# Performance work log

Measured on AMD Instinct MI355X. Metric: run time of the kernel, lower is better.

Reference implementation:

```python
import math
import jax, jax.numpy as jnp
import numpy as np

NH = 16          # num attention heads
NOPE = 128       # qk_nope_head_dim
ROPE = 64        # qk_rope_head_dim
VD = 128         # v_head_dim
QLR = 1536       # q_lora_rank
IH = 8           # index_n_heads
ID = 128         # index_head_dim
TOPK = 8         # index_topk
EPS = 1e-5


def layernorm(x, w, b):
    mu = jnp.mean(x, axis=-1, keepdims=True)
    var = jnp.mean((x - mu) ** 2, axis=-1, keepdims=True)
    return (x - mu) * jax.lax.rsqrt(var + EPS) * w + b


def rope_tables(dim, end, base=10000.0):
    freqs = 1.0 / (base ** (jnp.arange(0, dim, 2, dtype=jnp.float32) / dim))  # [dim//2]
    t = jnp.arange(end, dtype=jnp.float32)
    f = jnp.outer(t, freqs)  # [end, dim//2]
    return jnp.cos(f), jnp.sin(f)


def apply_rope(x, cos, sin):
    # x: [b, h, s, d]; cos/sin: [s, d//2] (interleaved real/imag pairs)
    xr, xi = x[..., 0::2], x[..., 1::2]
    c = cos[None, None, :, :]
    s = sin[None, None, :, :]
    or_, oi = xr * c - xi * s, xr * s + xi * c
    return jnp.stack([or_, oi], axis=-1).reshape(x.shape)


def setup_inputs() -> dict:
    key = jax.random.key(0)
    ks = jax.random.split(key, 16)
    H = 2048
    B, S = 2, 2048
    w = lambda k, shp: (jax.random.normal(k, shp, dtype=jnp.float32) * 0.02)
    return {
        "x": jax.random.normal(ks[0], (B, S, H), dtype=jnp.float32),
        "W_cq": w(ks[1], (H, QLR)),
        "q_norm_w": jnp.ones((QLR,), jnp.float32),
        "q_norm_b": jnp.zeros((QLR,), jnp.float32),
        "W_q": w(ks[2], (QLR, NH * (NOPE + ROPE))),
        "W_ckv": w(ks[3], (H, NH * (NOPE + ROPE))),
        "kv_norm_w": jnp.ones((NOPE,), jnp.float32),
        "kv_norm_b": jnp.zeros((NOPE,), jnp.float32),
        "W_kv": w(ks[4], (NOPE, NOPE + VD)),
        "W_o": w(ks[5], (NH * VD, H)),
        "W_ip": w(ks[6], (H, IH * ID)),
        "W_ig": w(ks[7], (H, IH)),
        "W_sq": w(ks[8], (ID, ID)),
        "W_sk": w(ks[9], (ID, ID)),
        "W_sv": w(ks[10], (ID, ID)),
        "W_io": w(ks[11], (ID, H)),
    }


def _forward(x, W_cq, q_norm_w, q_norm_b, W_q, W_ckv, kv_norm_w, kv_norm_b,
             W_kv, W_o, W_ip, W_ig, W_sq, W_sk, W_sv, W_io):
    B, S, H = x.shape
    # --- MLA dense path ---
    qc = layernorm(x @ W_cq, q_norm_w, q_norm_b)                  # [B,S,QLR]
    qp = (qc @ W_q).reshape(B, S, NH, NOPE + ROPE).transpose(0, 2, 1, 3)
    q_nope, q_pe = qp[..., :NOPE], qp[..., NOPE:]
    kvc = (x @ W_ckv).reshape(B, S, NH, ROPE + NOPE).transpose(0, 2, 1, 3)
    k_pe, kv_nope = kvc[..., :ROPE], kvc[..., ROPE:]
    kv_n = layernorm(kv_nope, kv_norm_w, kv_norm_b)               # [B,NH,S,NOPE]
    kvp = kv_n @ W_kv                                             # [B,NH,S,NOPE+VD]
    k_nope, v = kvp[..., :NOPE], kvp[..., NOPE:]
    cos, sin = rope_tables(ROPE, S)
    q_pe = apply_rope(q_pe, cos, sin)
    k_pe = apply_rope(k_pe, cos, sin)
    q = jnp.concatenate([q_nope, q_pe], axis=-1)                  # [B,NH,S,192]
    k = jnp.concatenate([k_nope, k_pe], axis=-1)
    scale = 1.0 / math.sqrt(NOPE + ROPE)
    scores = jnp.einsum("bhqd,bhkd->bhqk", q, k) * scale
    causal = jnp.triu(jnp.ones((S, S), dtype=bool), k=1)
    scores = jnp.where(causal[None, None], -jnp.inf, scores)
    probs = jax.nn.softmax(scores.astype(jnp.float32), axis=-1).astype(q.dtype)
    attn = jnp.einsum("bhqk,bhkd->bhqd", probs, v)                # [B,NH,S,VD]
    # --- NSA sparse path (lightning indexer) ---
    ist = (x @ W_ip).reshape(B, S, IH, ID).transpose(0, 2, 1, 3)  # [B,IH,S,ID]
    gate = (x @ W_ig).transpose(0, 2, 1)                          # [B,IH,S]
    _, top_idx = jax.lax.top_k(gate, TOPK)                        # [B,IH,TOPK]
    sel = jnp.take_along_axis(ist, top_idx[..., None], axis=2)    # [B,IH,TOPK,ID]
    sq, sk, sv = sel @ W_sq, sel @ W_sk, sel @ W_sv
    ss = jnp.einsum("bhqd,bhkd->bhqk", sq, sk) / math.sqrt(ID)    # [B,IH,TOPK,TOPK]
    sp = jax.nn.softmax(ss.astype(jnp.float32), axis=-1).astype(sq.dtype)
    so = jnp.einsum("bhqk,bhkd->bhqd", sp, sv)                    # [B,IH,TOPK,ID]
    sparse_out = so @ W_io                                        # [B,IH,TOPK,H]
    io = sparse_out.mean(axis=2)[:, :, None, :VD]                 # [B,IH,1,VD]
    io = jnp.broadcast_to(io, (B, IH, S, VD))
    io = jnp.repeat(io, NH // IH, axis=1)                         # [B,NH,S,VD]
    attn = attn + io
    out = attn.transpose(0, 2, 1, 3).reshape(B, S, NH * VD) @ W_o
    return out


def reference(x, W_cq, q_norm_w, q_norm_b, W_q, W_ckv, kv_norm_w, kv_norm_b,
              W_kv, W_o, W_ip, W_ig, W_sq, W_sk, W_sv, W_io):
    return _forward(x, W_cq, q_norm_w, q_norm_b, W_q, W_ckv, kv_norm_w,
                    kv_norm_b, W_kv, W_o, W_ip, W_ig, W_sq, W_sk, W_sv, W_io)
```

## Files before the change

kernel.cpp:

```cpp
#include <hip/hip_runtime.h>
#include <hip/hip_bf16.h>
#include <math.h>

#define NH    16
#define NOPE  128
#define ROPED 64
#define VD    128
#define QLR   1536
#define IH    8
#define ID    128
#define TOPK  8
#define EPSF  1e-5f
#define B_    2
#define S_    2048
#define H_    2048

using bf16 = __hip_bfloat16;
typedef __attribute__((ext_vector_type(8))) short short8;
typedef __attribute__((ext_vector_type(4))) short short4v;
typedef __attribute__((ext_vector_type(4))) float f32x4;

#define GLOBAL_AS __attribute__((address_space(1)))
#define LDS_AS    __attribute__((address_space(3)))

__device__ __forceinline__ float b2f(bf16 v) { return __bfloat162float(v); }
__device__ __forceinline__ bf16 f2b(float v) { return __float2bfloat16(v); }
__device__ __forceinline__ void stoC(float* p, float v) { *p = v; }
__device__ __forceinline__ void stoC(bf16* p, float v) { *p = __float2bfloat16(v); }

__global__ __launch_bounds__(256) void gate_k(const float* __restrict__ x,
                                              const float* __restrict__ Wg,
                                              float* __restrict__ gate) {
    const int t = threadIdx.x;
    const int wid = t >> 6, lane = t & 63;
    const int row = blockIdx.x * 4 + wid;
    const float* xp = x + (size_t)row * H_;

    float acc[8] = {};
    for (int k0 = 0; k0 < H_; k0 += 256) {
        const int kb = k0 + lane * 4;
        const f32x4 xv = *(const f32x4*)(xp + kb);
        const f32x4 w0 = *(const f32x4*)(Wg + (size_t)kb * 8);
        const f32x4 w1 = *(const f32x4*)(Wg + (size_t)kb * 8 + 4);
        const f32x4 w2 = *(const f32x4*)(Wg + (size_t)(kb + 1) * 8);
        const f32x4 w3 = *(const f32x4*)(Wg + (size_t)(kb + 1) * 8 + 4);
        const f32x4 w4 = *(const f32x4*)(Wg + (size_t)(kb + 2) * 8);
        const f32x4 w5 = *(const f32x4*)(Wg + (size_t)(kb + 2) * 8 + 4);
        const f32x4 w6 = *(const f32x4*)(Wg + (size_t)(kb + 3) * 8);
        const f32x4 w7 = *(const f32x4*)(Wg + (size_t)(kb + 3) * 8 + 4);
#pragma unroll
        for (int j = 0; j < 4; j++) {
            acc[j]     += xv[0] * w0[j] + xv[1] * w2[j] + xv[2] * w4[j] + xv[3] * w6[j];
            acc[4 + j] += xv[0] * w1[j] + xv[1] * w3[j] + xv[2] * w5[j] + xv[3] * w7[j];
        }
    }
#pragma unroll
    for (int j = 0; j < 8; j++) {
#pragma unroll
        for (int off = 32; off > 0; off >>= 1)
            acc[j] += __shfl_xor(acc[j], off);
    }
    if (lane == 0) {
#pragma unroll
        for (int j = 0; j < 8; j++) gate[(size_t)row * 8 + j] = acc[j];
    }
}

template <typename OT>
__global__ __launch_bounds__(256) void gemm_bt_mfma_k(const bf16* __restrict__ A,
                                                      const bf16* __restrict__ Bt,
                                                      OT* __restrict__ C,
                                                      int M, int N, int K) {
    __shared__ bf16 As[128 * 32];
    __shared__ bf16 Bs[128 * 32];
    const int t = threadIdx.x;
    const int w = t >> 6;
    const int l = t & 63;
    const int col = l & 15;
    const int quad = l >> 4;
    const int wm = w >> 1, wn = w & 1;
    const int row0 = blockIdx.y * 128;
    const int col0 = blockIdx.x * 128;

    const int rA = l >> 2;
    const int cA = (l & 3) * 8;
    const bf16* ga0 = A + (size_t)(row0 + w * 16 + rA) * K + cA;
    const bf16* ga1 = A + (size_t)(row0 + (4 + w) * 16 + rA) * K + cA;
    const bf16* gb0 = Bt + (size_t)(col0 + w * 16 + rA) * K + cA;
    const bf16* gb1 = Bt + (size_t)(col0 + (4 + w) * 16 + rA) * K + cA;
    bf16* lA0 = &As[w * 512];
    bf16* lA1 = &As[(4 + w) * 512];
    bf16* lB0 = &Bs[w * 512];
    bf16* lB1 = &Bs[(4 + w) * 512];

    f32x4 acc[4][4];
#pragma unroll
    for (int i = 0; i < 4; i++)
#pragma unroll
        for (int j = 0; j < 4; j++) acc[i][j] = (f32x4){0.f, 0.f, 0.f, 0.f};

    for (int k0 = 0; k0 < K; k0 += 32) {
        __syncthreads();
        __builtin_amdgcn_global_load_lds((const GLOBAL_AS void*)(ga0 + k0),
                                         (LDS_AS void*)lA0, 16, 0, 0);
        __builtin_amdgcn_global_load_lds((const GLOBAL_AS void*)(ga1 + k0),
                                         (LDS_AS void*)lA1, 16, 0, 0);
        __builtin_amdgcn_global_load_lds((const GLOBAL_AS void*)(gb0 + k0),
                                         (LDS_AS void*)lB0, 16, 0, 0);
        __builtin_amdgcn_global_load_lds((const GLOBAL_AS void*)(gb1 + k0),
                                         (LDS_AS void*)lB1, 16, 0, 0);
        __syncthreads();

        short8 af[4], bfr[4];
#pragma unroll
        for (int i = 0; i < 4; i++) {
            af[i]  = *(const short8*)&As[(wm * 64 + i * 16 + col) * 32 + quad * 8];
            bfr[i] = *(const short8*)&Bs[(wn * 64 + i * 16 + col) * 32 + quad * 8];
        }
#pragma unroll
        for (int i = 0; i < 4; i++)
#pragma unroll
            for (int j = 0; j < 4; j++)
                acc[i][j] = __builtin_amdgcn_mfma_f32_16x16x32_bf16(af[i], bfr[j], acc[i][j], 0, 0, 0);
    }

#pragma unroll
    for (int i = 0; i < 4; i++)
#pragma unroll
        for (int j = 0; j < 4; j++)
#pragma unroll
            for (int r = 0; r < 4; r++) {
                const int gr = row0 + wm * 64 + i * 16 + quad * 4 + r;
                const int gc = col0 + wn * 64 + j * 16 + col;
                stoC(C + (size_t)gr * N + gc, acc[i][j][r]);
            }
}

__global__ __launch_bounds__(256) void gemm_kv_k(const bf16* __restrict__ A,
                                                 const bf16* __restrict__ Bt,
                                                 bf16* __restrict__ kvc,
                                                 bf16* __restrict__ Vb) {
    __shared__ bf16 As[128 * 32];
    __shared__ bf16 Bs[128 * 32];
    const int K = 128;
    const int t = threadIdx.x;
    const int w = t >> 6;
    const int l = t & 63;
    const int col = l & 15;
    const int quad = l >> 4;
    const int wm = w >> 1, wn = w & 1;
    const int row0 = blockIdx.y * 128;
    const int col0 = blockIdx.x * 128;

    const int rA = l >> 2;
    const int cA = (l & 3) * 8;
    const bf16* ga0 = A + (size_t)(row0 + w * 16 + rA) * K + cA;
    const bf16* ga1 = A + (size_t)(row0 + (4 + w) * 16 + rA) * K + cA;
    const bf16* gb0 = Bt + (size_t)(col0 + w * 16 + rA) * K + cA;
    const bf16* gb1 = Bt + (size_t)(col0 + (4 + w) * 16 + rA) * K + cA;
    bf16* lA0 = &As[w * 512];
    bf16* lA1 = &As[(4 + w) * 512];
    bf16* lB0 = &Bs[w * 512];
    bf16* lB1 = &Bs[(4 + w) * 512];

    f32x4 acc[4][4];
#pragma unroll
    for (int i = 0; i < 4; i++)
#pragma unroll
        for (int j = 0; j < 4; j++) acc[i][j] = (f32x4){0.f, 0.f, 0.f, 0.f};

    for (int k0 = 0; k0 < K; k0 += 32) {
        __syncthreads();
        __builtin_amdgcn_global_load_lds((const GLOBAL_AS void*)(ga0 + k0),
                                         (LDS_AS void*)lA0, 16, 0, 0);
        __builtin_amdgcn_global_load_lds((const GLOBAL_AS void*)(ga1 + k0),
                                         (LDS_AS void*)lA1, 16, 0, 0);
        __builtin_amdgcn_global_load_lds((const GLOBAL_AS void*)(gb0 + k0),
                                         (LDS_AS void*)lB0, 16, 0, 0);
        __builtin_amdgcn_global_load_lds((const GLOBAL_AS void*)(gb1 + k0),
                                         (LDS_AS void*)lB1, 16, 0, 0);
        __syncthreads();

        short8 af[4], bfr[4];
#pragma unroll
        for (int i = 0; i < 4; i++) {
            af[i]  = *(const short8*)&As[(wm * 64 + i * 16 + col) * 32 + quad * 8];
            bfr[i] = *(const short8*)&Bs[(wn * 64 + i * 16 + col) * 32 + quad * 8];
        }
#pragma unroll
        for (int i = 0; i < 4; i++)
#pragma unroll
            for (int j = 0; j < 4; j++)
                acc[i][j] = __builtin_amdgcn_mfma_f32_16x16x32_bf16(af[i], bfr[j], acc[i][j], 0, 0, 0);
    }

#pragma unroll
    for (int i = 0; i < 4; i++)
#pragma unroll
        for (int j = 0; j < 4; j++)
#pragma unroll
            for (int r = 0; r < 4; r++) {
                const int gr = row0 + wm * 64 + i * 16 + quad * 4 + r;
                const int gc = col0 + wn * 64 + j * 16 + col;
                const int bb = gr >> 15;
                const int ss = (gr >> 4) & (S_ - 1);
                const int hh = gr & (NH - 1);
                const bf16 v = f2b(acc[i][j][r]);
                if (gc < 128) kvc[(size_t)gr * 192 + gc] = v;
                else Vb[(((size_t)(bb * NH + hh)) * S_ + ss) * 128 + (gc - 128)] = v;
            }
}

__global__ __launch_bounds__(256) void kv_ln_k(bf16* __restrict__ kvc,
                                               const float* __restrict__ knw,
                                               const float* __restrict__ knb,
                                               bf16* __restrict__ kvn) {
    const int idx = blockIdx.x * 4 + (threadIdx.x >> 6);
    const int lane = threadIdx.x & 63;
    const int s = (idx >> 4) & (S_ - 1);
    const size_t base = (size_t)idx * 192;

    const float v0 = b2f(kvc[base + 64 + lane]);
    const float v1 = b2f(kvc[base + 128 + lane]);
    float xr = 0.f, xi = 0.f;
    if (lane < 32) { xr = b2f(kvc[base + 2 * lane]); xi = b2f(kvc[base + 2 * lane + 1]); }

    float s1 = v0 + v1, s2 = v0 * v0 + v1 * v1;
#pragma unroll
    for (int off = 32; off > 0; off >>= 1) {
        s1 += __shfl_xor(s1, off);
        s2 += __shfl_xor(s2, off);
    }
    const float mu = s1 * (1.f / 128.f);
    const float rinv = rsqrtf(s2 * (1.f / 128.f) - mu * mu + EPSF);
    kvn[(size_t)idx * 128 + lane]      = f2b((v0 - mu) * rinv * knw[lane] + knb[lane]);
    kvn[(size_t)idx * 128 + lane + 64] = f2b((v1 - mu) * rinv * knw[lane + 64] + knb[lane + 64]);

    if (lane < 32) {
        const float freq = powf(10000.f, -(float)(2 * lane) / 64.f);
        const float ang = (float)s * freq;
        float sn, c; sincosf(ang, &sn, &c);
        kvc[base + 128 + 2 * lane]     = f2b(xr * c - xi * sn);
        kvc[base + 128 + 2 * lane + 1] = f2b(xr * sn + xi * c);
    }
}

__global__ __launch_bounds__(256) void cast_bf16_k(const float* __restrict__ X,
                                                   bf16* __restrict__ Y, int n4) {
    for (int i = blockIdx.x * 256 + threadIdx.x; i < n4; i += gridDim.x * 256) {
        const f32x4 v = ((const f32x4*)X)[i];
        short4v o;
#pragma unroll
        for (int j = 0; j < 4; j++) {
            bf16 b = f2b(v[j]);
            o[j] = *(short*)&b;
        }
        ((short4v*)Y)[i] = o;
    }
}

__global__ __launch_bounds__(256) void transpose_cast_k(const float* __restrict__ W,
                                                        bf16* __restrict__ Wt,
                                                        int K, int N) {
    __shared__ float tile[32][33];
    const int t = threadIdx.x;
    const int tx = t & 31, ty = t >> 5;
    const int n0 = blockIdx.x * 32;
    const int k0 = blockIdx.y * 32;
#pragma unroll
    for (int i = 0; i < 4; i++)
        tile[ty + 8 * i][tx] = W[(size_t)(k0 + ty + 8 * i) * N + n0 + tx];
    __syncthreads();
#pragma unroll
    for (int i = 0; i < 4; i++)
        Wt[(size_t)(n0 + ty + 8 * i) * K + k0 + tx] = f2b(tile[tx][ty + 8 * i]);
}

__global__ __launch_bounds__(256) void layernorm_cast_k(const float* __restrict__ X,
                                                        const float* __restrict__ w,
                                                        const float* __restrict__ b,
                                                        bf16* __restrict__ Y,
                                                        int L) {
    __shared__ float r1[256], r2[256];
    const int row = blockIdx.x;
    const int t = threadIdx.x;
    const float* xp = X + (size_t)row * L;
    bf16* yp = Y + (size_t)row * L;
    float s1 = 0.f, s2 = 0.f;
    for (int j = t; j < L; j += 256) { const float v = xp[j]; s1 += v; s2 += v * v; }
    r1[t] = s1; r2[t] = s2; __syncthreads();
    for (int off = 128; off > 0; off >>= 1) {
        if (t < off) { r1[t] += r1[t + off]; r2[t] += r2[t + off]; }
        __syncthreads();
    }
    const float mu   = r1[0] / (float)L;
    const float var  = r2[0] / (float)L - mu * mu;
    const float rinv = rsqrtf(var + EPSF);
    for (int j = t; j < L; j += 256)
        yp[j] = f2b((xp[j] - mu) * rinv * w[j] + b[j]);
}

__global__ __launch_bounds__(256) void q_rope_k(bf16* __restrict__ qp) {
    const int total = B_ * S_ * NH * 32;
    for (int p = blockIdx.x * 256 + threadIdx.x; p < total; p += gridDim.x * 256) {
        const int j = p & 31;
        const int row = p >> 5;
        const int sr = row >> 4;
        const int s = sr & (S_ - 1);
        const size_t base = (size_t)row * 192 + 128 + 2 * j;
        const float xr = b2f(qp[base]);
        const float xi = b2f(qp[base + 1]);
        const float freq = powf(10000.f, -(float)(2 * j) / 64.f);
        const float ang = (float)s * freq;
        float sn, c; sincosf(ang, &sn, &c);
        qp[base]     = f2b(xr * c - xi * sn);
        qp[base + 1] = f2b(xr * sn + xi * c);
    }
}

__global__ __launch_bounds__(256) void sparse_k(const float* __restrict__ gate,
                                                const float* __restrict__ ist,
                                                const float* __restrict__ Wsq,
                                                const float* __restrict__ Wsk,
                                                const float* __restrict__ Wsv,
                                                const float* __restrict__ Wio,
                                                float* __restrict__ io) {
    __shared__ float g[S_];
    __shared__ float sel[TOPK][ID];
    __shared__ float sq[TOPK][ID], sk[TOPK][ID], sv[TOPK][ID];
    __shared__ float sp[TOPK][TOPK];
    __shared__ float ms[ID];
    __shared__ float rv[256];
    __shared__ int ri[256];
    __shared__ int sidx[TOPK];
    const int bi = blockIdx.x;
    const int ih = bi % IH;
    const int b = bi / IH;
    const int t = threadIdx.x;

    for (int s = t; s < S_; s += 256) g[s] = gate[(size_t)(b * S_ + s) * IH + ih];
    __syncthreads();

    for (int r = 0; r < TOPK; r++) {
        float bv = -INFINITY; int bx = S_;
        for (int s = t; s < S_; s += 256) {
            const float v = g[s];
            if (v > bv) { bv = v; bx = s; }
        }
        rv[t] = bv; ri[t] = bx; __syncthreads();
        for (int off = 128; off > 0; off >>= 1) {
            if (t < off) {
                const float v2 = rv[t + off]; const int i2 = ri[t + off];
                if (v2 > rv[t] || (v2 == rv[t] && i2 < ri[t])) { rv[t] = v2; ri[t] = i2; }
            }
            __syncthreads();
        }
        if (t == 0) { sidx[r] = ri[0]; g[ri[0]] = -INFINITY; }
        __syncthreads();
    }

    for (int i = t; i < TOPK * ID; i += 256) {
        const int r = i >> 7, d = i & 127;
        sel[r][d] = ist[((size_t)(b * S_ + sidx[r]) * IH + ih) * ID + d];
    }
    __syncthreads();

    for (int i = t; i < TOPK * ID; i += 256) {
        const int r = i >> 7, n = i & 127;
        float aq = 0.f, ak = 0.f, av = 0.f;
        for (int k = 0; k < 128; k++) {
            const float s = sel[r][k];
            aq += s * Wsq[k * ID + n];
            ak += s * Wsk[k * ID + n];
            av += s * Wsv[k * ID + n];
        }
        sq[r][n] = aq; sk[r][n] = ak; sv[r][n] = av;
    }
    __syncthreads();

    if (t < TOPK * TOPK) {
        const int r = t >> 3, c = t & 7;
        float a = 0.f;
        for (int k = 0; k < 128; k++) a += sq[r][k] * sk[c][k];
        sp[r][c] = a * 0.08838834764831845f;
    }
    __syncthreads();

    if (t < TOPK) {
        float m = -INFINITY;
        for (int c = 0; c < 8; c++) m = fmaxf(m, sp[t][c]);
        float e[8]; float sum = 0.f;
        for (int c = 0; c < 8; c++) { e[c] = expf(sp[t][c] - m); sum += e[c]; }
        for (int c = 0; c < 8; c++) sp[t][c] = e[c] / sum;
    }
    __syncthreads();

    if (t < ID) {
        float acc = 0.f;
        for (int r = 0; r < 8; r++) {
            float so = 0.f;
            for (int c = 0; c < 8; c++) so += sp[r][c] * sv[c][t];
            acc += so;
        }
        ms[t] = acc * 0.125f;
    }
    __syncthreads();

    if (t < ID) {
        float acc = 0.f;
        for (int k = 0; k < 128; k++) acc += ms[k] * Wio[(size_t)k * H_ + t];
        io[((size_t)b * IH + ih) * ID + t] = acc;
    }
}

__global__ __launch_bounds__(256) void attn_mfma_k(const bf16* __restrict__ Qp,
                                                   const bf16* __restrict__ Kc,
                                                   const bf16* __restrict__ Vb,
                                                   const float* __restrict__ io,
                                                   bf16* __restrict__ O) {
    __shared__ unsigned short Kt[64 * 200];
    __shared__ unsigned short Vt[128 * 72];
    __shared__ unsigned short Ps[4 * 16 * 72];
    __shared__ float io_s[128];

    const int lin = blockIdx.x + 16 * blockIdx.y + 256 * blockIdx.z;
    const int swz = (lin & 7) * 64 + (lin >> 3);
    const int pairi = swz & 15;
    const int h = (swz >> 4) & 15;
    const int b = swz >> 8;

    const int t = threadIdx.x;
    const int lane = t & 63;
    const int wq = t >> 6;
    const int col = lane & 15;
    const int quad = lane >> 4;

    if (t < 128) io_s[t] = io[((size_t)b * IH + (h >> 1)) * ID + t];

    const float scale = 0.07216878364870322f;

#pragma unroll 1
    for (int ti = 0; ti < 2; ti++) {
        const int qt = (ti == 0) ? pairi : 31 - pairi;
        const int q0 = qt * 64;

        short8 qfrag[6];
        {
            const int q = q0 + wq * 16 + col;
            const short8* qrow = (const short8*)(Qp + ((size_t)(b * S_ + q) * NH + h) * 192);
#pragma unroll
            for (int kc = 0; kc < 6; kc++) qfrag[kc] = qrow[kc * 4 + quad];
        }

        float m_r[4], l_r[4];
#pragma unroll
        for (int r = 0; r < 4; r++) { m_r[r] = -1e30f; l_r[r] = 0.f; }
        f32x4 accO[8];
#pragma unroll
        for (int nt = 0; nt < 8; nt++) accO[nt] = (f32x4){0.f, 0.f, 0.f, 0.f};

        const int nkt = qt + 1;

        for (int kt = 0; kt < nkt; kt++) {
            const int kt0 = kt * 64;
            __syncthreads();
            {
                const int kr = t >> 2;
                const int c0 = (t & 3) * 48;
                const short8* src = (const short8*)(Kc + ((size_t)(b * S_ + kt0 + kr) * NH + h) * 192 + c0);
                short8* dst = (short8*)&Kt[kr * 200 + c0];
#pragma unroll
                for (int c = 0; c < 6; c++) dst[c] = src[c];
            }
            {
                const int ki = t >> 2;
                const short8* vsrc = (const short8*)(Vb + ((size_t)(b * NH + h) * S_ + kt0 + ki) * 128);
                short8 vv[4];
#pragma unroll
                for (int c = 0; c < 4; c++) vv[c] = vsrc[(t & 3) * 4 + c];
#pragma unroll
                for (int c = 0; c < 4; c++)
#pragma unroll
                    for (int e = 0; e < 8; e++) {
                        const int dv = (t & 3) * 32 + c * 8 + e;
                        Vt[dv * 72 + ki] = (unsigned short)vv[c][e];
                    }
            }
            __syncthreads();

            f32x4 s[4];
            __builtin_amdgcn_s_setprio(1);
#pragma unroll
            for (int nt = 0; nt < 4; nt++) {
                f32x4 acc = (f32x4){0.f, 0.f, 0.f, 0.f};
#pragma unroll
                for (int kc = 0; kc < 6; kc++) {
                    const short8 kf = *(const short8*)&Kt[(nt * 16 + col) * 200 + kc * 32 + quad * 8];
                    acc = __builtin_amdgcn_mfma_f32_16x16x32_bf16(qfrag[kc], kf, acc, 0, 0, 0);
                }
                s[nt] = acc;
            }
            __builtin_amdgcn_s_setprio(0);
#pragma unroll
            for (int nt = 0; nt < 4; nt++)
#pragma unroll
                for (int r = 0; r < 4; r++) {
                    const int kg = kt0 + nt * 16 + col;
                    const int qg = q0 + wq * 16 + quad * 4 + r;
                    const float v = s[nt][r] * scale;
                    s[nt][r] = (kg > qg) ? -1e30f : v;
                }
            float alpha[4];
#pragma unroll
            for (int r = 0; r < 4; r++) {
                float mt = fmaxf(fmaxf(s[0][r], s[1][r]), fmaxf(s[2][r], s[3][r]));
                mt = fmaxf(mt, __shfl_xor(mt, 1));
                mt = fmaxf(mt, __shfl_xor(mt, 2));
                mt = fmaxf(mt, __shfl_xor(mt, 4));
                mt = fmaxf(mt, __shfl_xor(mt, 8));
                const float mn = fmaxf(m_r[r], mt);
                alpha[r] = __expf(m_r[r] - mn);
                m_r[r] = mn;
                float rs = 0.f;
#pragma unroll
                for (int nt = 0; nt < 4; nt++) {
                    const float p = __expf(s[nt][r] - mn);
                    s[nt][r] = p;
                    rs += p;
                }
                rs += __shfl_xor(rs, 1);
                rs += __shfl_xor(rs, 2);
                rs += __shfl_xor(rs, 4);
                rs += __shfl_xor(rs, 8);
                l_r[r] = l_r[r] * alpha[r] + rs;
            }
            {
                unsigned short* pw = &Ps[wq * 1152];
#pragma unroll
                for (int nt = 0; nt < 4; nt++)
#pragma unroll
                    for (int r = 0; r < 4; r++) {
                        bf16 hv = f2b(s[nt][r]);
                        pw[(quad * 4 + r) * 72 + nt * 16 + col] = *(unsigned short*)&hv;
                    }
            }
            short8 pf[2];
#pragma unroll
            for (int kk = 0; kk < 2; kk++)
                pf[kk] = *(const short8*)&Ps[wq * 1152 + col * 72 + kk * 32 + quad * 8];
#pragma unroll
            for (int nt = 0; nt < 8; nt++)
#pragma unroll
                for (int r = 0; r < 4; r++) accO[nt][r] *= alpha[r];
            __builtin_amdgcn_s_setprio(1);
#pragma unroll
            for (int nt = 0; nt < 8; nt++) {
#pragma unroll
                for (int kk = 0; kk < 2; kk++) {
                    const short8 vf = *(const short8*)&Vt[(nt * 16 + col) * 72 + kk * 32 + quad * 8];
                    accO[nt] = __builtin_amdgcn_mfma_f32_16x16x32_bf16(pf[kk], vf, accO[nt], 0, 0, 0);
                }
            }
            __builtin_amdgcn_s_setprio(0);
        }

        float rinv[4];
#pragma unroll
        for (int r = 0; r < 4; r++) rinv[r] = 1.f / l_r[r];
#pragma unroll
        for (int nt = 0; nt < 8; nt++) {
            const int dv = nt * 16 + col;
            const float iov = io_s[dv];
#pragma unroll
            for (int r = 0; r < 4; r++) {
                const int q = q0 + wq * 16 + quad * 4 + r;
                O[((size_t)(b * S_ + q) * NH + h) * VD + dv] = f2b(accO[nt][r] * rinv[r] + iov);
            }
        }
    }
}

extern "C" void kernel_launch(void* const* d_in, const int* in_sizes, int n_in,
                              void* d_out, int out_size, void* d_ws, size_t ws_size,
                              hipStream_t stream) {
    const float* x      = (const float*)d_in[0];
    const float* W_cq   = (const float*)d_in[1];
    const float* qn_w   = (const float*)d_in[2];
    const float* qn_b   = (const float*)d_in[3];
    const float* W_q    = (const float*)d_in[4];
    const float* W_ckv  = (const float*)d_in[5];
    const float* kvn_w  = (const float*)d_in[6];
    const float* kvn_b  = (const float*)d_in[7];
    const float* W_kv   = (const float*)d_in[8];
    const float* W_o    = (const float*)d_in[9];
    const float* W_ip   = (const float*)d_in[10];
    const float* W_ig   = (const float*)d_in[11];
    const float* W_sq   = (const float*)d_in[12];
    const float* W_sk   = (const float*)d_in[13];
    const float* W_sv   = (const float*)d_in[14];
    const float* W_io   = (const float*)d_in[15];
    float* out = (float*)d_out;

    const int M = B_ * S_;

    char* wsb = (char*)d_ws;
    float* rbig  = (float*)wsb;
    bf16*  kvn   = (bf16*)(wsb + 16777216);
    bf16*  qp    = (bf16*)(wsb + 33554432);
    bf16*  kvc   = (bf16*)(wsb + 58720256);
    bf16*  cqb   = (bf16*)(wsb + 58720256);
    bf16*  Vb    = (bf16*)(wsb + 83886080);
    bf16*  Wt    = (bf16*)(wsb + 83886080);
    float* gate  = (float*)(wsb + 100663296);
    bf16*  WkvT  = (bf16*)(wsb + 100663296);
    float* iob   = (float*)(wsb + 100794368);
    float* cq    = rbig;
    float* ist   = rbig;
    bf16*  attnb = (bf16*)rbig;
    bf16*  xb    = (bf16*)d_out;

    dim3 blk(256);

    cast_bf16_k<<<dim3(2048), blk, 0, stream>>>(x, xb, M * H_ / 4);

    transpose_cast_k<<<dim3(QLR / 32, H_ / 32), blk, 0, stream>>>(W_cq, Wt, H_, QLR);
    gemm_bt_mfma_k<float><<<dim3(QLR / 128, M / 128), blk, 0, stream>>>(xb, Wt, cq, M, QLR, H_);
    layernorm_cast_k<<<dim3(M), blk, 0, stream>>>(cq, qn_w, qn_b, cqb, QLR);

    transpose_cast_k<<<dim3(3072 / 32, QLR / 32), blk, 0, stream>>>(W_q, Wt, QLR, 3072);
    gemm_bt_mfma_k<bf16><<<dim3(3072 / 128, M / 128), blk, 0, stream>>>(cqb, Wt, qp, M, 3072, QLR);

    transpose_cast_k<<<dim3(3072 / 32, H_ / 32), blk, 0, stream>>>(W_ckv, Wt, H_, 3072);
    gemm_bt_mfma_k<bf16><<<dim3(3072 / 128, M / 128), blk, 0, stream>>>(xb, Wt, kvc, M, 3072, H_);

    transpose_cast_k<<<dim3(1024 / 32, H_ / 32), blk, 0, stream>>>(W_ip, Wt, H_, 1024);
    gemm_bt_mfma_k<float><<<dim3(1024 / 128, M / 128), blk, 0, stream>>>(xb, Wt, ist, M, IH * ID, H_);

    gate_k<<<dim3(M / 4), blk, 0, stream>>>(x, W_ig, gate);

    q_rope_k<<<dim3(2048), blk, 0, stream>>>(qp);

    kv_ln_k<<<dim3(B_ * S_ * NH / 4), blk, 0, stream>>>(kvc, kvn_w, kvn_b, kvn);

    sparse_k<<<dim3(B_ * IH), blk, 0, stream>>>(gate, ist, W_sq, W_sk, W_sv, W_io, iob);

    transpose_cast_k<<<dim3(256 / 32, 128 / 32), blk, 0, stream>>>(W_kv, WkvT, 128, 256);
    gemm_kv_k<<<dim3(2, (B_ * S_ * NH) / 128), blk, 0, stream>>>(kvn, WkvT, kvc, Vb);

    attn_mfma_k<<<dim3(16, NH, B_), blk, 0, stream>>>(qp, kvc, Vb, iob, attnb);

    transpose_cast_k<<<dim3(H_ / 32, H_ / 32), blk, 0, stream>>>(W_o, Wt, H_, H_);
    gemm_bt_mfma_k<float><<<dim3(H_ / 128, M / 128), blk, 0, stream>>>(attnb, Wt, out, M, H_, H_);
}
```

Measured before the change: 722.8 us.

## Store V transposed from KV GEMM, remap GEMM blocks across XCDs, cheapen RoPE freq

The KV up-projection GEMM now writes V as a transposed [b,h,dv,s] plane with packed 4-element stores. The attention kernel can then load V tiles into LDS with straight vector copies instead of a scattered per-element transpose. Both GEMM kernels remap the linear block index so consecutive tiles land on the same XCD chiplet, aiming for better L2 reuse. RoPE frequency computation swaps powf for exp2f with a precomputed constant. The transposed V store is a strided write pattern that may cost some GEMM epilogue bandwidth.

```diff
diff --git a/kernel.cpp b/kernel.cpp
--- a/kernel.cpp
+++ b/kernel.cpp
@@ -79,8 +79,13 @@
     const int col = l & 15;
     const int quad = l >> 4;
     const int wm = w >> 1, wn = w & 1;
-    const int row0 = blockIdx.y * 128;
-    const int col0 = blockIdx.x * 128;
+
+    const int gx = gridDim.x;
+    const int nwg = gx * gridDim.y;
+    const int lin = blockIdx.y * gx + blockIdx.x;
+    const int work = (lin & 7) * (nwg >> 3) + (lin >> 3);
+    const int row0 = (work / gx) * 128;
+    const int col0 = (work % gx) * 128;
 
     const int rA = l >> 2;
     const int cA = (l & 3) * 8;
@@ -139,7 +144,7 @@
 __global__ __launch_bounds__(256) void gemm_kv_k(const bf16* __restrict__ A,
                                                  const bf16* __restrict__ Bt,
                                                  bf16* __restrict__ kvc,
-                                                 bf16* __restrict__ Vb) {
+                                                 bf16* __restrict__ VbT) {
     __shared__ bf16 As[128 * 32];
     __shared__ bf16 Bs[128 * 32];
     const int K = 128;
@@ -149,8 +154,13 @@
     const int col = l & 15;
     const int quad = l >> 4;
     const int wm = w >> 1, wn = w & 1;
-    const int row0 = blockIdx.y * 128;
-    const int col0 = blockIdx.x * 128;
+
+    const int gx = gridDim.x;
+    const int nwg = gx * gridDim.y;
+    const int lin = blockIdx.y * gx + blockIdx.x;
+    const int work = (lin & 7) * (nwg >> 3) + (lin >> 3);
+    const int row0 = (work / gx) * 128;
+    const int col0 = (work % gx) * 128;
 
     const int rA = l >> 2;
     const int cA = (l & 3) * 8;
@@ -194,21 +204,36 @@
                 acc[i][j] = __builtin_amdgcn_mfma_f32_16x16x32_bf16(af[i], bfr[j], acc[i][j], 0, 0, 0);
     }
 
-#pragma unroll
-    for (int i = 0; i < 4; i++)
-#pragma unroll
-        for (int j = 0; j < 4; j++)
+    if (col0 == 0) {
+#pragma unroll
+        for (int i = 0; i < 4; i++)
+#pragma unroll
+            for (int j = 0; j < 4; j++)
+#pragma unroll
+                for (int r = 0; r < 4; r++) {
+                    const int gr = row0 + wm * 64 + i * 16 + quad * 4 + r;
+                    const int gc = wn * 64 + j * 16 + col;
+                    kvc[(size_t)gr * 192 + gc] = f2b(acc[i][j][r]);
+                }
+    } else {
+        const int bb = row0 >> 15;
+        const int ssb = ((row0 >> 4) & (S_ - 1)) + wm * 4;
+#pragma unroll
+        for (int j = 0; j < 4; j++) {
+            const int dv = wn * 64 + j * 16 + col;
 #pragma unroll
             for (int r = 0; r < 4; r++) {
-                const int gr = row0 + wm * 64 + i * 16 + quad * 4 + r;
-                const int gc = col0 + wn * 64 + j * 16 + col;
-                const int bb = gr >> 15;
-                const int ss = (gr >> 4) & (S_ - 1);
-                const int hh = gr & (NH - 1);
-                const bf16 v = f2b(acc[i][j][r]);
-                if (gc < 128) kvc[(size_t)gr * 192 + gc] = v;
-                else Vb[(((size_t)(bb * NH + hh)) * S_ + ss) * 128 + (gc - 128)] = v;
-            }
+                const int hh = quad * 4 + r;
+                short4v pk;
+#pragma unroll
+                for (int i = 0; i < 4; i++) {
+                    bf16 v = f2b(acc[i][j][r]);
+                    pk[i] = *(short*)&v;
+                }
+                *(short4v*)&VbT[((size_t)(bb * NH + hh) * 128 + dv) * S_ + ssb] = pk;
+            }
+        }
+    }
 }
 
 __global__ __launch_bounds__(256) void kv_ln_k(bf16* __restrict__ kvc,
@@ -237,7 +262,7 @@
     kvn[(size_t)idx * 128 + lane + 64] = f2b((v1 - mu) * rinv * knw[lane + 64] + knb[lane + 64]);
 
     if (lane < 32) {
-        const float freq = powf(10000.f, -(float)(2 * lane) / 64.f);
+        const float freq = exp2f(-0.41524101186092014f * (float)lane);
         const float ang = (float)s * freq;
         float sn, c; sincosf(ang, &sn, &c);
         kvc[base + 128 + 2 * lane]     = f2b(xr * c - xi * sn);
@@ -310,7 +335,7 @@
         const size_t base = (size_t)row * 192 + 128 + 2 * j;
         const float xr = b2f(qp[base]);
         const float xi = b2f(qp[base + 1]);
-        const float freq = powf(10000.f, -(float)(2 * j) / 64.f);
+        const float freq = exp2f(-0.41524101186092014f * (float)j);
         const float ang = (float)s * freq;
         float sn, c; sincosf(ang, &sn, &c);
         qp[base]     = f2b(xr * c - xi * sn);
@@ -415,7 +440,7 @@
 
 __global__ __launch_bounds__(256) void attn_mfma_k(const bf16* __restrict__ Qp,
                                                    const bf16* __restrict__ Kc,
-                                                   const bf16* __restrict__ Vb,
+                                                   const bf16* __restrict__ VbT,
                                                    const float* __restrict__ io,
                                                    bf16* __restrict__ O) {
     __shared__ unsigned short Kt[64 * 200];
@@ -438,6 +463,7 @@
     if (t < 128) io_s[t] = io[((size_t)b * IH + (h >> 1)) * ID + t];
 
     const float scale = 0.07216878364870322f;
+    const bf16* vplane = VbT + (size_t)(b * NH + h) * 128 * (size_t)S_;
 
 #pragma unroll 1
     for (int ti = 0; ti < 2; ti++) {
@@ -473,18 +499,13 @@
                 for (int c = 0; c < 6; c++) dst[c] = src[c];
             }
             {
-                const int ki = t >> 2;
-                const short8* vsrc = (const short8*)(Vb + ((size_t)(b * NH + h) * S_ + kt0 + ki) * 128);
-                short8 vv[4];
-#pragma unroll
-                for (int c = 0; c < 4; c++) vv[c] = vsrc[(t & 3) * 4 + c];
-#pragma unroll
-                for (int c = 0; c < 4; c++)
-#pragma unroll
-                    for (int e = 0; e < 8; e++) {
-                        const int dv = (t & 3) * 32 + c * 8 + e;
-                        Vt[dv * 72 + ki] = (unsigned short)vv[c][e];
-                    }
+                const int ki0 = (t & 7) * 8;
+#pragma unroll
+                for (int p = 0; p < 4; p++) {
+                    const int dv = p * 32 + (t >> 3);
+                    const short8 vv = *(const short8*)(vplane + (size_t)dv * S_ + kt0 + ki0);
+                    *(short8*)&Vt[dv * 72 + ki0] = vv;
+                }
             }
             __syncthreads();
 
@@ -609,7 +630,7 @@
     bf16*  qp    = (bf16*)(wsb + 33554432);
     bf16*  kvc   = (bf16*)(wsb + 58720256);
     bf16*  cqb   = (bf16*)(wsb + 58720256);
-    bf16*  Vb    = (bf16*)(wsb + 83886080);
+    bf16*  VbT   = (bf16*)(wsb + 83886080);
     bf16*  Wt    = (bf16*)(wsb + 83886080);
     float* gate  = (float*)(wsb + 100663296);
     bf16*  WkvT  = (bf16*)(wsb + 100663296);
@@ -645,9 +666,9 @@
     sparse_k<<<dim3(B_ * IH), blk, 0, stream>>>(gate, ist, W_sq, W_sk, W_sv, W_io, iob);
 
     transpose_cast_k<<<dim3(256 / 32, 128 / 32), blk, 0, stream>>>(W_kv, WkvT, 128, 256);
-    gemm_kv_k<<<dim3(2, (B_ * S_ * NH) / 128), blk, 0, stream>>>(kvn, WkvT, kvc, Vb);
-
-    attn_mfma_k<<<dim3(16, NH, B_), blk, 0, stream>>>(qp, kvc, Vb, iob, attnb);
+    gemm_kv_k<<<dim3(2, (B_ * S_ * NH) / 128), blk, 0, stream>>>(kvn, WkvT, kvc, VbT);
+
+    attn_mfma_k<<<dim3(16, NH, B_), blk, 0, stream>>>(qp, kvc, VbT, iob, attnb);
 
     transpose_cast_k<<<dim3(H_ / 32, H_ / 32), blk, 0, stream>>>(W_o, Wt, H_, H_);
     gemm_bt_mfma_k<float><<<dim3(H_ / 128, M / 128), blk, 0, stream>>>(attnb, Wt, out, M, H_, H_);
```

Measured after the change: 685.1 us. 1.05x faster.
